# Performance work log

Hardware: AMD Instinct MI355X
Metric: run time of the kernel (lower is better)

## Reference

```python
import jax, jax.numpy as jnp
import numpy as np

B, S, D, H = 4, 2048, 1024, 16
DK = D // H
THETA = 10000.0


def _rope(x, sin, cos):
    # x: (B, H, S, DK) interleaved-pair RoPE
    x_even = x[..., 0::2]
    x_odd = x[..., 1::2]
    out_even = x_even * cos - x_odd * sin
    out_odd = x_odd * cos + x_even * sin
    return jnp.stack((out_even, out_odd), axis=-1).reshape(x.shape)


def setup_inputs() -> dict:
    key = jax.random.key(0)
    kx, kq, kk, kv, ko = jax.random.split(key, 5)
    std = np.sqrt(2.0 / (D + D)).astype(np.float32)
    return {
        "x": jax.random.normal(kx, (B, S, D), dtype=jnp.float32),
        "Wq": jax.random.normal(kq, (D, D), dtype=jnp.float32) * std,
        "Wk": jax.random.normal(kk, (D, D), dtype=jnp.float32) * std,
        "Wv": jax.random.normal(kv, (D, D), dtype=jnp.float32) * std,
        "Wo": jax.random.normal(ko, (D, D), dtype=jnp.float32) * std,
    }


def reference(x, Wq, Wk, Wv, Wo):
    # QKV projections: Linear has no bias, weight is (d_out, d_in)
    def proj(w):
        y = jnp.einsum("bsd,od->bso", x, w)
        return y.reshape(B, S, H, DK).transpose(0, 2, 1, 3)  # (B,H,S,DK)

    Q, K, V = proj(Wq), proj(Wk), proj(Wv)

    # RoPE angles for positions 0..S-1 (token_positions default = arange)
    k = jnp.arange(DK // 2, dtype=jnp.float32)
    inv_freq = 1.0 / (THETA ** (2.0 * k / DK))          # (DK/2,)
    angles = jnp.arange(S, dtype=jnp.float32)[:, None] * inv_freq  # (S, DK/2)
    sin, cos = jnp.sin(angles), jnp.cos(angles)

    Q = _rope(Q, sin, cos)
    K = _rope(K, sin, cos)

    scores = jnp.einsum("bhqd,bhkd->bhqk", Q, K) / jnp.sqrt(jnp.float32(DK))
    causal = jnp.tril(jnp.ones((S, S), dtype=bool))
    scores = jnp.where(causal, scores, -jnp.inf)
    probs = jax.nn.softmax(scores, axis=-1)

    attn = jnp.einsum("bhqk,bhkd->bhqd", probs, V)       # (B,H,S,DK)
    attn = attn.transpose(0, 2, 1, 3).reshape(B, S, D)
    return jnp.einsum("bsd,od->bso", attn, Wo)
```

## Files before the change

### kernel.cpp

```cpp
#include <hip/hip_runtime.h>
#include <stdint.h>

typedef unsigned short u16;
typedef unsigned int   u32;
typedef __bf16  bf16x8 __attribute__((ext_vector_type(8)));
typedef float   f32x4  __attribute__((ext_vector_type(4)));
typedef float   f32x16 __attribute__((ext_vector_type(16)));
typedef unsigned int u32x4 __attribute__((ext_vector_type(4)));

#define B_SZ   4
#define S_LEN  2048
#define D_DIM  1024
#define NH     16
#define DKH    64
#define M_ROWS (B_SZ * S_LEN)
#define GK     1024

#define C_SC 0.1803368801111204f

#define KVLOC(r, hf) ((((r) & 3)) + 8 * ((r) >> 2) + 4 * (hf))

static __device__ __forceinline__ u16 f2bf(float f) {
  return __builtin_bit_cast(u16, (__bf16)f);
}

static __device__ __forceinline__ u32 pk2(float lo, float hi) {
  ushort2 u = { f2bf(lo), f2bf(hi) };
  return __builtin_bit_cast(u32, u);
}

static __device__ __forceinline__ float fexp2(float x) {
  return __builtin_amdgcn_exp2f(x);
}

static __device__ __forceinline__ f32x4 mfma16(bf16x8 a, bf16x8 b, f32x4 c) {
  return __builtin_amdgcn_mfma_f32_16x16x32_bf16(a, b, c, 0, 0, 0);
}

static __device__ __forceinline__ f32x16 mfma32(bf16x8 a, bf16x8 b, f32x16 c) {
  return __builtin_amdgcn_mfma_f32_32x32x16_bf16(a, b, c, 0, 0, 0);
}

static __device__ __forceinline__ void gld_lds16(const u16* g, u16* l) {
  __builtin_amdgcn_global_load_lds(
      (const __attribute__((address_space(1))) u32*)g,
      (__attribute__((address_space(3))) u32*)l, 16, 0, 0);
}

static __device__ __forceinline__ void wg_barrier() {
  asm volatile("s_waitcnt lgkmcnt(0)" ::: "memory");
  __builtin_amdgcn_s_barrier();
  __builtin_amdgcn_sched_barrier(0);
}

#define SWZ(row, col) (((row) * 64) + (((col) ^ (((row) & 7) << 3))))

__global__ void k_cvt_all(const float* __restrict__ x,
                          const float* __restrict__ wq, const float* __restrict__ wk,
                          const float* __restrict__ wv, const float* __restrict__ wo,
                          u16* __restrict__ xb, u16* __restrict__ wqb,
                          u16* __restrict__ wkb, u16* __restrict__ wvb,
                          u16* __restrict__ wob, float2* __restrict__ tabT) {
  int bid = blockIdx.x;
  if (bid >= 12288) {
    int i = (bid - 12288) * 256 + threadIdx.x;
    int k = i >> 11, s = i & 2047;
    float freq = powf(10000.0f, -(float)k / 32.0f);
    float a = (float)s * freq;
    tabT[i] = make_float2(cosf(a), sinf(a));
    return;
  }
  const float* src; u16* dst; int base;
  if (bid < 8192) {
    src = x; dst = xb; base = bid;
  } else {
    int j = bid - 8192, sel = j >> 10;
    src = (sel == 0) ? wq : (sel == 1) ? wk : (sel == 2) ? wv : wo;
    dst = (sel == 0) ? wqb : (sel == 1) ? wkb : (sel == 2) ? wvb : wob;
    base = j & 1023;
  }
  int i = base * 256 + threadIdx.x;
  float4 v = reinterpret_cast<const float4*>(src)[i];
  ushort4 o = { f2bf(v.x), f2bf(v.y), f2bf(v.z), f2bf(v.w) };
  reinterpret_cast<ushort4*>(dst)[i] = o;
}

#define ASLOT 8192
#define BSLOT 8192

static __device__ __forceinline__ void g128_stage(
    const u16* __restrict__ A, const u16* __restrict__ B,
    int M0, int N0, int kt, u16* As, u16* Bs, int w, int lane) {
  const int lr = lane >> 3;
  const int lg = (lane & 7) ^ lr;
  const size_t k0 = (size_t)kt * 64;
  const int rb = w * 8 + lr;
#pragma unroll
  for (int p = 0; p < 2; ++p)
    gld_lds16(A + (size_t)(M0 + p * 64 + rb) * GK + k0 + lg * 8,
              As + (p * 64 + w * 8) * 64);
#pragma unroll
  for (int p = 0; p < 2; ++p)
    gld_lds16(B + (size_t)(N0 + p * 64 + rb) * GK + k0 + lg * 8,
              Bs + (p * 64 + w * 8) * 64);
}

static __device__ __forceinline__ void g128_loop(
    const u16* __restrict__ A, const u16* __restrict__ B,
    int M0, int N0, u16* As, u16* Bs, f32x4 acc[2][4], int w, int lane) {
  const int cl = lane & 15, gp = lane >> 4;
  const int wr = w >> 1, wc = w & 1;

  g128_stage(A, B, M0, N0, 0, As, Bs, w, lane);
  asm volatile("s_waitcnt vmcnt(0)" ::: "memory");
  __builtin_amdgcn_s_barrier();
  __builtin_amdgcn_sched_barrier(0);

#pragma unroll 1
  for (int kt = 0; kt < 16; ++kt) {
    const int s = kt & 1;
    if (kt + 1 < 16)
      g128_stage(A, B, M0, N0, kt + 1, As + (s ^ 1) * ASLOT,
                 Bs + (s ^ 1) * BSLOT, w, lane);

    const u16* As_ = As + s * ASLOT;
    const u16* Bs_ = Bs + s * BSLOT;
#pragma unroll
    for (int kk = 0; kk < 2; ++kk) {
      bf16x8 af[2], bfr[4];
#pragma unroll
      for (int m = 0; m < 2; ++m)
        af[m] = *reinterpret_cast<const bf16x8*>(
            &As_[SWZ(wr * 32 + m * 16 + cl, kk * 32 + gp * 8)]);
#pragma unroll
      for (int n = 0; n < 4; ++n)
        bfr[n] = *reinterpret_cast<const bf16x8*>(
            &Bs_[SWZ(wc * 64 + n * 16 + cl, kk * 32 + gp * 8)]);
      __builtin_amdgcn_s_setprio(1);
#pragma unroll
      for (int m = 0; m < 2; ++m)
#pragma unroll
        for (int n = 0; n < 4; ++n)
          acc[m][n] = mfma16(af[m], bfr[n], acc[m][n]);
      __builtin_amdgcn_s_setprio(0);
    }
    if (kt + 1 < 16) {
      asm volatile("s_waitcnt vmcnt(0)" ::: "memory");
      wg_barrier();
    }
  }
}

__global__ __launch_bounds__(512, 2)
void k_gemm_qkv2(const u16* __restrict__ Xb,
                 const u16* __restrict__ Wqb, const u16* __restrict__ Wkb,
                 const u16* __restrict__ Wvb,
                 const float2* __restrict__ tabT,
                 u16* __restrict__ Qr, u16* __restrict__ Kr,
                 u16* __restrict__ Vt) {
  __shared__ u16 As[2 * ASLOT];
  __shared__ u16 Bs[2 * BSLOT];
  const int tid = threadIdx.x, lane = tid & 63, w = tid >> 6;
  const int id = blockIdx.x;
  const int xcd = id & 7, rid = id >> 3;
  const int mt = (rid & 7) * 8 + xcd;
  const int np = rid >> 3;
  const int proj = np >> 3, nt = np & 7;
  const int M0 = mt * 128, N0 = nt * 128;
  const u16* W = (proj == 0) ? Wqb : (proj == 1) ? Wkb : Wvb;

  f32x4 zero = {0.f, 0.f, 0.f, 0.f};
  f32x4 acc[2][4];
#pragma unroll
  for (int m = 0; m < 2; ++m)
#pragma unroll
    for (int n = 0; n < 4; ++n) acc[m][n] = zero;

  g128_loop(Xb, W, M0, N0, As, Bs, acc, w, lane);

  const int cl = lane & 15, gp = lane >> 4;
  const int wr = w >> 1, wc = w & 1;

  if (proj < 2) {
    u16* dst = (proj == 0) ? Qr : Kr;
#pragma unroll
    for (int n = 0; n < 4; ++n) {
      int colo = N0 + wc * 64 + n * 16 + cl;
      int h = colo >> 6, dk = colo & 63;
      int kf = dk >> 1, par = dk & 1;
#pragma unroll
      for (int m = 0; m < 2; ++m) {
        int row0 = M0 + wr * 32 + m * 16 + gp * 4;
        int b = row0 >> 11, sp0 = row0 & (S_LEN - 1);
        const float4* tp = reinterpret_cast<const float4*>(&tabT[kf * 2048 + sp0]);
        float4 c01 = tp[0];
        float4 c23 = tp[1];
        float cs_c[4] = { c01.x, c01.z, c23.x, c23.z };
        float cs_s[4] = { c01.y, c01.w, c23.y, c23.w };
#pragma unroll
        for (int r = 0; r < 4; ++r) {
          float v = acc[m][n][r];
          float p = __shfl_xor(v, 1);
          float o = par ? (v * cs_c[r] + p * cs_s[r])
                        : (v * cs_c[r] - p * cs_s[r]);
          dst[((size_t)(b * NH + h) * S_LEN + sp0 + r) * DKH + dk] = f2bf(o);
        }
      }
    }
  } else {
#pragma unroll
    for (int m = 0; m < 2; ++m) {
#pragma unroll
      for (int n = 0; n < 4; ++n) {
        int colo = N0 + wc * 64 + n * 16 + cl;
        int h = colo >> 6, dk = colo & 63;
        int row0 = M0 + wr * 32 + m * 16 + gp * 4;
        int b = row0 >> 11, sp0 = row0 & (S_LEN - 1);
        ushort4 o4 = { f2bf(acc[m][n][0]), f2bf(acc[m][n][1]),
                       f2bf(acc[m][n][2]), f2bf(acc[m][n][3]) };
        *reinterpret_cast<ushort4*>(
            Vt + ((size_t)(b * NH + h) * DKH + dk) * S_LEN + sp0) = o4;
      }
    }
  }
}

__global__ __launch_bounds__(512, 2)
void k_gemm_out2(const u16* __restrict__ Ab, const u16* __restrict__ Wob,
                 float* __restrict__ out) {
  __shared__ u16 As[2 * ASLOT];
  __shared__ u16 Bs[2 * BSLOT];
  const int tid = threadIdx.x, lane = tid & 63, w = tid >> 6;
  const int id = blockIdx.x;
  const int xcd = id & 7, rid = id >> 3;
  const int mt = (rid & 7) * 8 + xcd;
  const int nt = rid >> 3;
  const int M0 = mt * 128, N0 = nt * 128;

  f32x4 zero = {0.f, 0.f, 0.f, 0.f};
  f32x4 acc[2][4];
#pragma unroll
  for (int m = 0; m < 2; ++m)
#pragma unroll
    for (int n = 0; n < 4; ++n) acc[m][n] = zero;

  g128_loop(Ab, Wob, M0, N0, As, Bs, acc, w, lane);

  const int cl = lane & 15, gp = lane >> 4;
  const int wr = w >> 1, wc = w & 1;
#pragma unroll
  for (int m = 0; m < 2; ++m)
#pragma unroll
    for (int n = 0; n < 4; ++n)
#pragma unroll
      for (int r = 0; r < 4; ++r) {
        int row = M0 + wr * 32 + m * 16 + gp * 4 + r;
        int col = N0 + wc * 64 + n * 16 + cl;
        out[(size_t)row * D_DIM + col] = acc[m][n][r];
      }
}

__global__ __launch_bounds__(256, 4)
void k_attn(const u16* __restrict__ Q, const u16* __restrict__ K,
            const u16* __restrict__ Vt, u16* __restrict__ Ob) {
  __shared__ u16 Ks[2][64 * 64];
  __shared__ u16 Vs[2][64 * 64];
  __shared__ float lbc[4][32];

  const int tid = threadIdx.x, lane = tid & 63, w = tid >> 6;
  const int rl = lane & 31, hf = lane >> 5;
  const int id   = blockIdx.x;
  const int xcd  = id & 7;
  const int g    = (id >> 3) & 7;
  const int p    = id >> 6;
  const int bh   = (xcd << 3) | g;
  const int qb   = (4 * (p & 3) + 5 * (p >> 2)) & 15;
  const u16* Qb = Q  + (size_t)bh * S_LEN * DKH;
  const u16* Kb = K  + (size_t)bh * S_LEN * DKH;
  const u16* Vb = Vt + (size_t)bh * DKH * S_LEN;
  const int b = bh >> 4, hd = bh & 15;

  const int lr = lane >> 3;
  const int lg = (lane & 7) ^ lr;
  const u16* kb_l = Kb + (w * 8 + lr) * DKH + lg * 8;
  const u16* vb_l = Vb + (size_t)(w * 8 + lr) * S_LEN + lg * 8;

#define STAGE(buf_, t_) do {                                                  \
    gld_lds16(kb_l + (size_t)(t_) * 64 * DKH,        &Ks[buf_][(w*8)*64]);    \
    gld_lds16(kb_l + (size_t)(t_) * 64 * DKH + 2048, &Ks[buf_][(32+w*8)*64]); \
    gld_lds16(vb_l + (size_t)(t_) * 64,              &Vs[buf_][(w*8)*64]);    \
    gld_lds16(vb_l + (size_t)(t_) * 64 + 32*S_LEN,   &Vs[buf_][(32+w*8)*64]); \
  } while (0)

  const int T    = 2 * qb + 2;
  const int qw32 = qb * 128 + w * 32;
  const int dwave = (qw32 + 31) >> 6;

  bf16x8 qf[4];
  {
    const u16* qp = Qb + (size_t)(qw32 + rl) * DKH + hf * 8;
#pragma unroll
    for (int s = 0; s < 4; ++s)
      qf[s] = *reinterpret_cast<const bf16x8*>(qp + s * 16);
  }

  f32x16 o0, o1;
#pragma unroll
  for (int r = 0; r < 16; ++r) { o0[r] = 0.f; o1[r] = 0.f; }
  float plr = 0.f;

  STAGE(0, 0);
  asm volatile("s_waitcnt vmcnt(0)" ::: "memory");
  __builtin_amdgcn_s_barrier();

  int cur = 0;
#pragma unroll 1
  for (int t = 0; t < T; ++t) {
    if (t + 1 < T) STAGE(cur ^ 1, t + 1);

    const bool act = (t <= dwave);

    if (act) {
      f32x16 s0, s1;
#pragma unroll
      for (int r = 0; r < 16; ++r) { s0[r] = 0.f; s1[r] = 0.f; }
      __builtin_amdgcn_s_setprio(1);
#pragma unroll
      for (int s = 0; s < 4; ++s) {
        bf16x8 k0 = *reinterpret_cast<const bf16x8*>(
            &Ks[cur][SWZ(rl,      s * 16 + hf * 8)]);
        bf16x8 k1 = *reinterpret_cast<const bf16x8*>(
            &Ks[cur][SWZ(32 + rl, s * 16 + hf * 8)]);
        s0 = mfma32(k0, qf[s], s0);
        s1 = mfma32(k1, qf[s], s1);
      }
      __builtin_amdgcn_s_setprio(0);

      if (t == dwave) {
        const int qrel = qw32 + rl - t * 64;
#pragma unroll
        for (int r = 0; r < 16; ++r) {
          const int kl = KVLOC(r, hf);
          if (kl > qrel)      s0[r] = -1e30f;
          if (32 + kl > qrel) s1[r] = -1e30f;
        }
      }

      float sv = 0.f;
      __builtin_amdgcn_s_setprio(1);
#pragma unroll
      for (int s = 0; s < 4; ++s) {
        const int r0 = (s & 1) * 8;
        float e0, e1, e2, e3, e4, e5, e6, e7;
        if (s < 2) {
          e0 = fexp2(s0[r0+0] * C_SC); e1 = fexp2(s0[r0+1] * C_SC);
          e2 = fexp2(s0[r0+2] * C_SC); e3 = fexp2(s0[r0+3] * C_SC);
          e4 = fexp2(s0[r0+4] * C_SC); e5 = fexp2(s0[r0+5] * C_SC);
          e6 = fexp2(s0[r0+6] * C_SC); e7 = fexp2(s0[r0+7] * C_SC);
        } else {
          e0 = fexp2(s1[r0+0] * C_SC); e1 = fexp2(s1[r0+1] * C_SC);
          e2 = fexp2(s1[r0+2] * C_SC); e3 = fexp2(s1[r0+3] * C_SC);
          e4 = fexp2(s1[r0+4] * C_SC); e5 = fexp2(s1[r0+5] * C_SC);
          e6 = fexp2(s1[r0+6] * C_SC); e7 = fexp2(s1[r0+7] * C_SC);
        }
        sv += ((e0 + e1) + (e2 + e3)) + ((e4 + e5) + (e6 + e7));
        u32x4 fw = { pk2(e0, e1), pk2(e2, e3), pk2(e4, e5), pk2(e6, e7) };
        bf16x8 af = __builtin_bit_cast(bf16x8, fw);
        uint2 va = *reinterpret_cast<const uint2*>(
            &Vs[cur][SWZ(rl,      s * 16 + 4 * hf)]);
        uint2 vb = *reinterpret_cast<const uint2*>(
            &Vs[cur][SWZ(rl,      s * 16 + 8 + 4 * hf)]);
        uint2 vc = *reinterpret_cast<const uint2*>(
            &Vs[cur][SWZ(32 + rl, s * 16 + 4 * hf)]);
        uint2 vd = *reinterpret_cast<const uint2*>(
            &Vs[cur][SWZ(32 + rl, s * 16 + 8 + 4 * hf)]);
        u32x4 v0w = { va.x, va.y, vb.x, vb.y };
        u32x4 v1w = { vc.x, vc.y, vd.x, vd.y };
        bf16x8 v0 = __builtin_bit_cast(bf16x8, v0w);
        bf16x8 v1 = __builtin_bit_cast(bf16x8, v1w);
        o0 = mfma32(af, v0, o0);
        o1 = mfma32(af, v1, o1);
      }
      __builtin_amdgcn_s_setprio(0);
      plr += sv;
    }

    asm volatile("s_waitcnt vmcnt(0)" ::: "memory");
    wg_barrier();
    cur ^= 1;
  }

  const float lsum = plr + __shfl_xor(plr, 32);
  lbc[w][rl] = 1.0f / lsum;
  asm volatile("s_waitcnt lgkmcnt(0)" ::: "memory");
#pragma unroll
  for (int r = 0; r < 16; ++r) {
    const float ivr = lbc[w][KVLOC(r, hf)];
    const int q = qw32 + KVLOC(r, hf);
    u16* op = Ob + ((size_t)(b * S_LEN + q)) * D_DIM + hd * DKH;
    op[rl]      = f2bf(o0[r] * ivr);
    op[32 + rl] = f2bf(o1[r] * ivr);
  }
#undef STAGE
}

extern "C" void kernel_launch(void* const* d_in, const int* in_sizes, int n_in,
                              void* d_out, int out_size, void* d_ws, size_t ws_size,
                              hipStream_t stream) {
  const float* x  = (const float*)d_in[0];
  const float* Wq = (const float*)d_in[1];
  const float* Wk = (const float*)d_in[2];
  const float* Wv = (const float*)d_in[3];
  const float* Wo = (const float*)d_in[4];
  float* out = (float*)d_out;

  char* ws = (char*)d_ws;
  size_t off = 0;
  u16* xb  = (u16*)(ws + off); off += (size_t)M_ROWS * D_DIM * 2;
  u16* wqb = (u16*)(ws + off); off += (size_t)D_DIM * D_DIM * 2;
  u16* wkb = (u16*)(ws + off); off += (size_t)D_DIM * D_DIM * 2;
  u16* wvb = (u16*)(ws + off); off += (size_t)D_DIM * D_DIM * 2;
  u16* wob = (u16*)(ws + off); off += (size_t)D_DIM * D_DIM * 2;
  float2* tab = (float2*)(ws + off); off += (size_t)S_LEN * 32 * 8;
  u16* Qr = (u16*)(ws + off); off += (size_t)M_ROWS * D_DIM * 2;
  u16* Kr = (u16*)(ws + off); off += (size_t)M_ROWS * D_DIM * 2;
  u16* Vt = (u16*)(ws + off); off += (size_t)M_ROWS * D_DIM * 2;
  u16* Ab = (u16*)(ws + off); off += (size_t)M_ROWS * D_DIM * 2;
  (void)ws_size; (void)in_sizes; (void)n_in; (void)out_size;

  k_cvt_all<<<12544, 256, 0, stream>>>(x, Wq, Wk, Wv, Wo,
                                       xb, wqb, wkb, wvb, wob, tab);

  k_gemm_qkv2<<<dim3(1536), 512, 0, stream>>>(xb, wqb, wkb, wvb, tab, Qr, Kr, Vt);
  k_attn<<<dim3(1024), 256, 0, stream>>>(Qr, Kr, Vt, Ab);
  k_gemm_out2<<<dim3(512), 512, 0, stream>>>(Ab, wob, out);
}
```

Measured before the change: 162.4 us.

## Restructure GEMM mainloop to 4-stage K=32 pipeline with two-ahead prefetch

Replaces the double-buffered K=64 GEMM mainloop with a 4-slot ring of K=32 stages, prefetching two stages ahead and waiting with a partial vmcnt so loads overlap more with MFMA work. It uses a new swizzle for 32-wide rows and halves LDS per stage while keeping total LDS the same. The cost is twice as many barriers per K step, and each barrier interval covers fewer MFMAs.

```diff
diff --git a/kernel.cpp b/kernel.cpp
--- a/kernel.cpp
+++ b/kernel.cpp
@@ -54,6 +54,7 @@
 }
 
 #define SWZ(row, col) (((row) * 64) + (((col) ^ (((row) & 7) << 3))))
+#define SWZ32(row, col) (((row) * 32) + (((col) ^ ((((row) >> 1) & 3) << 3))))
 
 __global__ void k_cvt_all(const float* __restrict__ x,
                           const float* __restrict__ wq, const float* __restrict__ wk,
@@ -85,67 +86,64 @@
   reinterpret_cast<ushort4*>(dst)[i] = o;
 }
 
-#define ASLOT 8192
-#define BSLOT 8192
-
-static __device__ __forceinline__ void g128_stage(
+#define SLOT32 4096
+
+static __device__ __forceinline__ void g32_stage(
     const u16* __restrict__ A, const u16* __restrict__ B,
-    int M0, int N0, int kt, u16* As, u16* Bs, int w, int lane) {
-  const int lr = lane >> 3;
-  const int lg = (lane & 7) ^ lr;
-  const size_t k0 = (size_t)kt * 64;
-  const int rb = w * 8 + lr;
-#pragma unroll
-  for (int p = 0; p < 2; ++p)
-    gld_lds16(A + (size_t)(M0 + p * 64 + rb) * GK + k0 + lg * 8,
-              As + (p * 64 + w * 8) * 64);
-#pragma unroll
-  for (int p = 0; p < 2; ++p)
-    gld_lds16(B + (size_t)(N0 + p * 64 + rb) * GK + k0 + lg * 8,
-              Bs + (p * 64 + w * 8) * 64);
-}
-
-static __device__ __forceinline__ void g128_loop(
+    int M0, int N0, int st, u16* As, u16* Bs, int w, int lane) {
+  const int row = lane >> 2;
+  const int cg  = (lane & 3) ^ ((lane >> 3) & 3);
+  const size_t k0 = (size_t)st * 32;
+  gld_lds16(A + (size_t)(M0 + w * 16 + row) * GK + k0 + cg * 8,
+            As + (w * 16) * 32);
+  gld_lds16(B + (size_t)(N0 + w * 16 + row) * GK + k0 + cg * 8,
+            Bs + (w * 16) * 32);
+}
+
+static __device__ __forceinline__ void g32_loop(
     const u16* __restrict__ A, const u16* __restrict__ B,
     int M0, int N0, u16* As, u16* Bs, f32x4 acc[2][4], int w, int lane) {
   const int cl = lane & 15, gp = lane >> 4;
   const int wr = w >> 1, wc = w & 1;
 
-  g128_stage(A, B, M0, N0, 0, As, Bs, w, lane);
-  asm volatile("s_waitcnt vmcnt(0)" ::: "memory");
+  g32_stage(A, B, M0, N0, 0, As + 0 * SLOT32, Bs + 0 * SLOT32, w, lane);
+  g32_stage(A, B, M0, N0, 1, As + 1 * SLOT32, Bs + 1 * SLOT32, w, lane);
+  asm volatile("s_waitcnt vmcnt(2)" ::: "memory");
   __builtin_amdgcn_s_barrier();
   __builtin_amdgcn_sched_barrier(0);
 
 #pragma unroll 1
-  for (int kt = 0; kt < 16; ++kt) {
-    const int s = kt & 1;
-    if (kt + 1 < 16)
-      g128_stage(A, B, M0, N0, kt + 1, As + (s ^ 1) * ASLOT,
-                 Bs + (s ^ 1) * BSLOT, w, lane);
-
-    const u16* As_ = As + s * ASLOT;
-    const u16* Bs_ = Bs + s * BSLOT;
-#pragma unroll
-    for (int kk = 0; kk < 2; ++kk) {
-      bf16x8 af[2], bfr[4];
-#pragma unroll
-      for (int m = 0; m < 2; ++m)
-        af[m] = *reinterpret_cast<const bf16x8*>(
-            &As_[SWZ(wr * 32 + m * 16 + cl, kk * 32 + gp * 8)]);
+  for (int ss = 0; ss < 32; ++ss) {
+    const int s = ss & 3;
+    if (ss + 2 < 32)
+      g32_stage(A, B, M0, N0, ss + 2,
+                As + ((ss + 2) & 3) * SLOT32, Bs + ((ss + 2) & 3) * SLOT32,
+                w, lane);
+
+    const u16* As_ = As + s * SLOT32;
+    const u16* Bs_ = Bs + s * SLOT32;
+    bf16x8 af[2], bfr[4];
+#pragma unroll
+    for (int m = 0; m < 2; ++m)
+      af[m] = *reinterpret_cast<const bf16x8*>(
+          &As_[SWZ32(wr * 32 + m * 16 + cl, gp * 8)]);
+#pragma unroll
+    for (int n = 0; n < 4; ++n)
+      bfr[n] = *reinterpret_cast<const bf16x8*>(
+          &Bs_[SWZ32(wc * 64 + n * 16 + cl, gp * 8)]);
+    __builtin_amdgcn_s_setprio(1);
+#pragma unroll
+    for (int m = 0; m < 2; ++m)
 #pragma unroll
       for (int n = 0; n < 4; ++n)
-        bfr[n] = *reinterpret_cast<const bf16x8*>(
-            &Bs_[SWZ(wc * 64 + n * 16 + cl, kk * 32 + gp * 8)]);
-      __builtin_amdgcn_s_setprio(1);
-#pragma unroll
-      for (int m = 0; m < 2; ++m)
-#pragma unroll
-        for (int n = 0; n < 4; ++n)
-          acc[m][n] = mfma16(af[m], bfr[n], acc[m][n]);
-      __builtin_amdgcn_s_setprio(0);
-    }
-    if (kt + 1 < 16) {
-      asm volatile("s_waitcnt vmcnt(0)" ::: "memory");
+        acc[m][n] = mfma16(af[m], bfr[n], acc[m][n]);
+    __builtin_amdgcn_s_setprio(0);
+
+    if (ss + 1 < 32) {
+      if (ss + 2 < 32)
+        asm volatile("s_waitcnt vmcnt(2)" ::: "memory");
+      else
+        asm volatile("s_waitcnt vmcnt(0)" ::: "memory");
       wg_barrier();
     }
   }
@@ -158,8 +156,8 @@
                  const float2* __restrict__ tabT,
                  u16* __restrict__ Qr, u16* __restrict__ Kr,
                  u16* __restrict__ Vt) {
-  __shared__ u16 As[2 * ASLOT];
-  __shared__ u16 Bs[2 * BSLOT];
+  __shared__ u16 As[4 * SLOT32];
+  __shared__ u16 Bs[4 * SLOT32];
   const int tid = threadIdx.x, lane = tid & 63, w = tid >> 6;
   const int id = blockIdx.x;
   const int xcd = id & 7, rid = id >> 3;
@@ -176,7 +174,7 @@
 #pragma unroll
     for (int n = 0; n < 4; ++n) acc[m][n] = zero;
 
-  g128_loop(Xb, W, M0, N0, As, Bs, acc, w, lane);
+  g32_loop(Xb, W, M0, N0, As, Bs, acc, w, lane);
 
   const int cl = lane & 15, gp = lane >> 4;
   const int wr = w >> 1, wc = w & 1;
@@ -228,8 +226,8 @@
 __global__ __launch_bounds__(512, 2)
 void k_gemm_out2(const u16* __restrict__ Ab, const u16* __restrict__ Wob,
                  float* __restrict__ out) {
-  __shared__ u16 As[2 * ASLOT];
-  __shared__ u16 Bs[2 * BSLOT];
+  __shared__ u16 As[4 * SLOT32];
+  __shared__ u16 Bs[4 * SLOT32];
   const int tid = threadIdx.x, lane = tid & 63, w = tid >> 6;
   const int id = blockIdx.x;
   const int xcd = id & 7, rid = id >> 3;
@@ -244,7 +242,7 @@
 #pragma unroll
     for (int n = 0; n < 4; ++n) acc[m][n] = zero;
 
-  g128_loop(Ab, Wob, M0, N0, As, Bs, acc, w, lane);
+  g32_loop(Ab, Wob, M0, N0, As, Bs, acc, w, lane);
 
   const int cl = lane & 15, gp = lane >> 4;
   const int wr = w >> 1, wc = w & 1;
```

Result: slower. 175.7 us (+8.2%).

## Fuse Q/K/V projections into one GEMM block sharing the X tile

Applied to the files above, without the earlier changes.

Each QKV GEMM block now computes the Q, K and V outputs for the same 128x128 tile. The X tile is loaded once per K-step and reused against three weight tiles, so the grid shrinks from 1536 to 512 blocks and X traffic drops by about a factor of three. The K-step is narrowed to 32 with a new swizzle to fit three B tiles in LDS. Launch bounds now ask for 4 blocks per CU, but holding three accumulator sets raises register pressure, and there are fewer blocks to spread across the CUs.

```diff
diff --git a/kernel.cpp b/kernel.cpp
--- a/kernel.cpp
+++ b/kernel.cpp
@@ -54,6 +54,7 @@
 }
 
 #define SWZ(row, col) (((row) * 64) + (((col) ^ (((row) & 7) << 3))))
+#define SWZ32(row, col) (((row) * 32) + (((col) ^ ((((row) >> 1) & 3) << 3))))
 
 __global__ void k_cvt_all(const float* __restrict__ x,
                           const float* __restrict__ wq, const float* __restrict__ wk,
@@ -85,104 +86,116 @@
   reinterpret_cast<ushort4*>(dst)[i] = o;
 }
 
-#define ASLOT 8192
-#define BSLOT 8192
-
-static __device__ __forceinline__ void g128_stage(
-    const u16* __restrict__ A, const u16* __restrict__ B,
-    int M0, int N0, int kt, u16* As, u16* Bs, int w, int lane) {
-  const int lr = lane >> 3;
-  const int lg = (lane & 7) ^ lr;
-  const size_t k0 = (size_t)kt * 64;
-  const int rb = w * 8 + lr;
-#pragma unroll
-  for (int p = 0; p < 2; ++p)
-    gld_lds16(A + (size_t)(M0 + p * 64 + rb) * GK + k0 + lg * 8,
-              As + (p * 64 + w * 8) * 64);
-#pragma unroll
-  for (int p = 0; p < 2; ++p)
-    gld_lds16(B + (size_t)(N0 + p * 64 + rb) * GK + k0 + lg * 8,
-              Bs + (p * 64 + w * 8) * 64);
-}
-
-static __device__ __forceinline__ void g128_loop(
-    const u16* __restrict__ A, const u16* __restrict__ B,
-    int M0, int N0, u16* As, u16* Bs, f32x4 acc[2][4], int w, int lane) {
-  const int cl = lane & 15, gp = lane >> 4;
-  const int wr = w >> 1, wc = w & 1;
-
-  g128_stage(A, B, M0, N0, 0, As, Bs, w, lane);
-  asm volatile("s_waitcnt vmcnt(0)" ::: "memory");
-  __builtin_amdgcn_s_barrier();
-  __builtin_amdgcn_sched_barrier(0);
-
-#pragma unroll 1
-  for (int kt = 0; kt < 16; ++kt) {
-    const int s = kt & 1;
-    if (kt + 1 < 16)
-      g128_stage(A, B, M0, N0, kt + 1, As + (s ^ 1) * ASLOT,
-                 Bs + (s ^ 1) * BSLOT, w, lane);
-
-    const u16* As_ = As + s * ASLOT;
-    const u16* Bs_ = Bs + s * BSLOT;
-#pragma unroll
-    for (int kk = 0; kk < 2; ++kk) {
-      bf16x8 af[2], bfr[4];
-#pragma unroll
-      for (int m = 0; m < 2; ++m)
-        af[m] = *reinterpret_cast<const bf16x8*>(
-            &As_[SWZ(wr * 32 + m * 16 + cl, kk * 32 + gp * 8)]);
-#pragma unroll
-      for (int n = 0; n < 4; ++n)
-        bfr[n] = *reinterpret_cast<const bf16x8*>(
-            &Bs_[SWZ(wc * 64 + n * 16 + cl, kk * 32 + gp * 8)]);
-      __builtin_amdgcn_s_setprio(1);
-#pragma unroll
-      for (int m = 0; m < 2; ++m)
-#pragma unroll
-        for (int n = 0; n < 4; ++n)
-          acc[m][n] = mfma16(af[m], bfr[n], acc[m][n]);
-      __builtin_amdgcn_s_setprio(0);
-    }
-    if (kt + 1 < 16) {
-      asm volatile("s_waitcnt vmcnt(0)" ::: "memory");
-      wg_barrier();
-    }
-  }
-}
-
-__global__ __launch_bounds__(512, 2)
+#define FSLOT 4096
+
+__global__ __launch_bounds__(512, 4)
 void k_gemm_qkv2(const u16* __restrict__ Xb,
                  const u16* __restrict__ Wqb, const u16* __restrict__ Wkb,
                  const u16* __restrict__ Wvb,
                  const float2* __restrict__ tabT,
                  u16* __restrict__ Qr, u16* __restrict__ Kr,
                  u16* __restrict__ Vt) {
-  __shared__ u16 As[2 * ASLOT];
-  __shared__ u16 Bs[2 * BSLOT];
+  __shared__ u16 As[2 * FSLOT];
+  __shared__ u16 Bs[2 * 3 * FSLOT];
   const int tid = threadIdx.x, lane = tid & 63, w = tid >> 6;
   const int id = blockIdx.x;
   const int xcd = id & 7, rid = id >> 3;
   const int mt = (rid & 7) * 8 + xcd;
-  const int np = rid >> 3;
-  const int proj = np >> 3, nt = np & 7;
+  const int nt = rid >> 3;
   const int M0 = mt * 128, N0 = nt * 128;
-  const u16* W = (proj == 0) ? Wqb : (proj == 1) ? Wkb : Wvb;
-
-  f32x4 zero = {0.f, 0.f, 0.f, 0.f};
-  f32x4 acc[2][4];
-#pragma unroll
-  for (int m = 0; m < 2; ++m)
-#pragma unroll
-    for (int n = 0; n < 4; ++n) acc[m][n] = zero;
-
-  g128_loop(Xb, W, M0, N0, As, Bs, acc, w, lane);
+
+  const int srow = lane >> 2;
+  const int scg  = (lane & 3) ^ ((lane >> 3) & 3);
+  const u16* a_l = Xb  + (size_t)(M0 + w * 16 + srow) * GK + scg * 8;
+  const u16* q_l = Wqb + (size_t)(N0 + w * 16 + srow) * GK + scg * 8;
+  const u16* k_l = Wkb + (size_t)(N0 + w * 16 + srow) * GK + scg * 8;
+  const u16* v_l = Wvb + (size_t)(N0 + w * 16 + srow) * GK + scg * 8;
+  u16* aL = As + (w * 16) * 32;
+
+#define FSTAGE(slot_, ss_) do {                                              \
+    const size_t k0_ = (size_t)(ss_) * 32;                                   \
+    gld_lds16(a_l + k0_, aL + (slot_) * FSLOT);                              \
+    gld_lds16(q_l + k0_, Bs + ((slot_) * 3 + 0) * FSLOT + (w * 16) * 32);    \
+    gld_lds16(k_l + k0_, Bs + ((slot_) * 3 + 1) * FSLOT + (w * 16) * 32);    \
+    gld_lds16(v_l + k0_, Bs + ((slot_) * 3 + 2) * FSLOT + (w * 16) * 32);    \
+  } while (0)
 
   const int cl = lane & 15, gp = lane >> 4;
   const int wr = w >> 1, wc = w & 1;
 
-  if (proj < 2) {
-    u16* dst = (proj == 0) ? Qr : Kr;
+  f32x4 zero = {0.f, 0.f, 0.f, 0.f};
+  f32x4 aQ[2][4], aK[2][4], aV[2][4];
+#pragma unroll
+  for (int m = 0; m < 2; ++m)
+#pragma unroll
+    for (int n = 0; n < 4; ++n) { aQ[m][n] = zero; aK[m][n] = zero; aV[m][n] = zero; }
+
+  FSTAGE(0, 0);
+  asm volatile("s_waitcnt vmcnt(0)" ::: "memory");
+  __builtin_amdgcn_s_barrier();
+  __builtin_amdgcn_sched_barrier(0);
+
+#pragma unroll 1
+  for (int ss = 0; ss < 32; ++ss) {
+    const int s = ss & 1;
+    if (ss + 1 < 32) FSTAGE(s ^ 1, ss + 1);
+
+    const u16* As_ = As + s * FSLOT;
+    bf16x8 af[2];
+#pragma unroll
+    for (int m = 0; m < 2; ++m)
+      af[m] = *reinterpret_cast<const bf16x8*>(
+          &As_[SWZ32(wr * 32 + m * 16 + cl, gp * 8)]);
+
+    __builtin_amdgcn_s_setprio(1);
+    {
+      const u16* B_ = Bs + (s * 3 + 0) * FSLOT;
+      bf16x8 bf[4];
+#pragma unroll
+      for (int n = 0; n < 4; ++n)
+        bf[n] = *reinterpret_cast<const bf16x8*>(
+            &B_[SWZ32(wc * 64 + n * 16 + cl, gp * 8)]);
+#pragma unroll
+      for (int m = 0; m < 2; ++m)
+#pragma unroll
+        for (int n = 0; n < 4; ++n) aQ[m][n] = mfma16(af[m], bf[n], aQ[m][n]);
+    }
+    {
+      const u16* B_ = Bs + (s * 3 + 1) * FSLOT;
+      bf16x8 bf[4];
+#pragma unroll
+      for (int n = 0; n < 4; ++n)
+        bf[n] = *reinterpret_cast<const bf16x8*>(
+            &B_[SWZ32(wc * 64 + n * 16 + cl, gp * 8)]);
+#pragma unroll
+      for (int m = 0; m < 2; ++m)
+#pragma unroll
+        for (int n = 0; n < 4; ++n) aK[m][n] = mfma16(af[m], bf[n], aK[m][n]);
+    }
+    {
+      const u16* B_ = Bs + (s * 3 + 2) * FSLOT;
+      bf16x8 bf[4];
+#pragma unroll
+      for (int n = 0; n < 4; ++n)
+        bf[n] = *reinterpret_cast<const bf16x8*>(
+            &B_[SWZ32(wc * 64 + n * 16 + cl, gp * 8)]);
+#pragma unroll
+      for (int m = 0; m < 2; ++m)
+#pragma unroll
+        for (int n = 0; n < 4; ++n) aV[m][n] = mfma16(af[m], bf[n], aV[m][n]);
+    }
+    __builtin_amdgcn_s_setprio(0);
+
+    if (ss + 1 < 32) {
+      asm volatile("s_waitcnt vmcnt(0)" ::: "memory");
+      wg_barrier();
+    }
+  }
+#undef FSTAGE
+
+#pragma unroll
+  for (int pj = 0; pj < 2; ++pj) {
+    u16* dst = (pj == 0) ? Qr : Kr;
 #pragma unroll
     for (int n = 0; n < 4; ++n) {
       int colo = N0 + wc * 64 + n * 16 + cl;
@@ -199,7 +212,7 @@
         float cs_s[4] = { c01.y, c01.w, c23.y, c23.w };
 #pragma unroll
         for (int r = 0; r < 4; ++r) {
-          float v = acc[m][n][r];
+          float v = (pj == 0) ? aQ[m][n][r] : aK[m][n][r];
           float p = __shfl_xor(v, 1);
           float o = par ? (v * cs_c[r] + p * cs_s[r])
                         : (v * cs_c[r] - p * cs_s[r]);
@@ -207,20 +220,85 @@
         }
       }
     }
-  } else {
-#pragma unroll
-    for (int m = 0; m < 2; ++m) {
-#pragma unroll
-      for (int n = 0; n < 4; ++n) {
-        int colo = N0 + wc * 64 + n * 16 + cl;
-        int h = colo >> 6, dk = colo & 63;
-        int row0 = M0 + wr * 32 + m * 16 + gp * 4;
-        int b = row0 >> 11, sp0 = row0 & (S_LEN - 1);
-        ushort4 o4 = { f2bf(acc[m][n][0]), f2bf(acc[m][n][1]),
-                       f2bf(acc[m][n][2]), f2bf(acc[m][n][3]) };
-        *reinterpret_cast<ushort4*>(
-            Vt + ((size_t)(b * NH + h) * DKH + dk) * S_LEN + sp0) = o4;
-      }
+  }
+#pragma unroll
+  for (int m = 0; m < 2; ++m) {
+#pragma unroll
+    for (int n = 0; n < 4; ++n) {
+      int colo = N0 + wc * 64 + n * 16 + cl;
+      int h = colo >> 6, dk = colo & 63;
+      int row0 = M0 + wr * 32 + m * 16 + gp * 4;
+      int b = row0 >> 11, sp0 = row0 & (S_LEN - 1);
+      ushort4 o4 = { f2bf(aV[m][n][0]), f2bf(aV[m][n][1]),
+                     f2bf(aV[m][n][2]), f2bf(aV[m][n][3]) };
+      *reinterpret_cast<ushort4*>(
+          Vt + ((size_t)(b * NH + h) * DKH + dk) * S_LEN + sp0) = o4;
+    }
+  }
+}
+
+#define ASLOT 8192
+#define BSLOT 8192
+
+static __device__ __forceinline__ void g128_stage(
+    const u16* __restrict__ A, const u16* __restrict__ B,
+    int M0, int N0, int kt, u16* As, u16* Bs, int w, int lane) {
+  const int lr = lane >> 3;
+  const int lg = (lane & 7) ^ lr;
+  const size_t k0 = (size_t)kt * 64;
+  const int rb = w * 8 + lr;
+#pragma unroll
+  for (int p = 0; p < 2; ++p)
+    gld_lds16(A + (size_t)(M0 + p * 64 + rb) * GK + k0 + lg * 8,
+              As + (p * 64 + w * 8) * 64);
+#pragma unroll
+  for (int p = 0; p < 2; ++p)
+    gld_lds16(B + (size_t)(N0 + p * 64 + rb) * GK + k0 + lg * 8,
+              Bs + (p * 64 + w * 8) * 64);
+}
+
+static __device__ __forceinline__ void g128_loop(
+    const u16* __restrict__ A, const u16* __restrict__ B,
+    int M0, int N0, u16* As, u16* Bs, f32x4 acc[2][4], int w, int lane) {
+  const int cl = lane & 15, gp = lane >> 4;
+  const int wr = w >> 1, wc = w & 1;
+
+  g128_stage(A, B, M0, N0, 0, As, Bs, w, lane);
+  asm volatile("s_waitcnt vmcnt(0)" ::: "memory");
+  __builtin_amdgcn_s_barrier();
+  __builtin_amdgcn_sched_barrier(0);
+
+#pragma unroll 1
+  for (int kt = 0; kt < 16; ++kt) {
+    const int s = kt & 1;
+    if (kt + 1 < 16)
+      g128_stage(A, B, M0, N0, kt + 1, As + (s ^ 1) * ASLOT,
+                 Bs + (s ^ 1) * BSLOT, w, lane);
+
+    const u16* As_ = As + s * ASLOT;
+    const u16* Bs_ = Bs + s * BSLOT;
+#pragma unroll
+    for (int kk = 0; kk < 2; ++kk) {
+      bf16x8 af[2], bfr[4];
+#pragma unroll
+      for (int m = 0; m < 2; ++m)
+        af[m] = *reinterpret_cast<const bf16x8*>(
+            &As_[SWZ(wr * 32 + m * 16 + cl, kk * 32 + gp * 8)]);
+#pragma unroll
+      for (int n = 0; n < 4; ++n)
+        bfr[n] = *reinterpret_cast<const bf16x8*>(
+            &Bs_[SWZ(wc * 64 + n * 16 + cl, kk * 32 + gp * 8)]);
+      __builtin_amdgcn_s_setprio(1);
+#pragma unroll
+      for (int m = 0; m < 2; ++m)
+#pragma unroll
+        for (int n = 0; n < 4; ++n)
+          acc[m][n] = mfma16(af[m], bfr[n], acc[m][n]);
+      __builtin_amdgcn_s_setprio(0);
+    }
+    if (kt + 1 < 16) {
+      asm volatile("s_waitcnt vmcnt(0)" ::: "memory");
+      wg_barrier();
     }
   }
 }
@@ -431,7 +509,7 @@
   k_cvt_all<<<12544, 256, 0, stream>>>(x, Wq, Wk, Wv, Wo,
                                        xb, wqb, wkb, wvb, wob, tab);
 
-  k_gemm_qkv2<<<dim3(1536), 512, 0, stream>>>(xb, wqb, wkb, wvb, tab, Qr, Kr, Vt);
+  k_gemm_qkv2<<<dim3(512), 512, 0, stream>>>(xb, wqb, wkb, wvb, tab, Qr, Kr, Vt);
   k_attn<<<dim3(1024), 256, 0, stream>>>(Qr, Kr, Vt, Ab);
   k_gemm_out2<<<dim3(512), 512, 0, stream>>>(Ab, wob, out);
 }
```

After: 234.0 us. 1.44x slower.
